# Kernel optimization log

Hardware: AMD Instinct MI355X
Metric: run time of the kernel (lower is better)

Reference implementation:

```python
import jax, jax.numpy as jnp
import numpy as np

B, S, D = 8, 1024, 768
H, DK = 12, 64
DFF = 3072
EPS = 1e-5


def setup_inputs() -> dict:
    key = jax.random.key(0)
    ks = jax.random.split(key, 12)
    s = lambda fan_in: 1.0 / np.sqrt(fan_in)
    return {
        "x": jax.random.normal(ks[0], (B, S, D), jnp.float32),
        "Wq": jax.random.normal(ks[1], (D, D), jnp.float32) * s(D),
        "Wk": jax.random.normal(ks[2], (D, D), jnp.float32) * s(D),
        "Wv": jax.random.normal(ks[3], (D, D), jnp.float32) * s(D),
        "Wo": jax.random.normal(ks[4], (D, D), jnp.float32) * s(D),
        "g1": jnp.ones((D,), jnp.float32),
        "b1": jnp.zeros((D,), jnp.float32),
        "g2": jnp.ones((D,), jnp.float32),
        "b2": jnp.zeros((D,), jnp.float32),
        "W1": jax.random.normal(ks[5], (D, DFF), jnp.float32) * s(D),
        "bW1": jnp.zeros((DFF,), jnp.float32),
        "W2": jax.random.normal(ks[6], (DFF, D), jnp.float32) * s(DFF),
        "bW2": jnp.zeros((D,), jnp.float32),
    }


def _layernorm(x, g, b):
    mu = x.mean(-1, keepdims=True)
    var = ((x - mu) ** 2).mean(-1, keepdims=True)
    return (x - mu) * jax.lax.rsqrt(var + EPS) * g + b


def reference(x, Wq, Wk, Wv, Wo, g1, b1, g2, b2, W1, bW1, W2, bW2):
    scale = DK ** (-0.5)
    # pre-norm attention block
    h = _layernorm(x, g1, b1)
    q = (h @ Wq).reshape(B, S, H, DK)
    k = (h @ Wk).reshape(B, S, H, DK)
    v = (h @ Wv).reshape(B, S, H, DK)
    logits = jnp.einsum("bqhd,bkhd->bhqk", q, k) * scale  # [B,H,S,S]
    weights = jax.nn.softmax(logits, axis=-1)
    attn = jnp.einsum("bhqk,bkhd->bqhd", weights, v).reshape(B, S, D)
    x = x + attn @ Wo
    # pre-norm FFN block
    h = _layernorm(x, g2, b2)
    h = jax.nn.gelu(h @ W1 + bW1, approximate=False)
    x = x + h @ W2 + bW2
    return x
```

## Files before the change

### kernel.cpp

```cpp
#include <hip/hip_runtime.h>
#include <cstdint>
#include <cstddef>

#define B_   8
#define S_   1024
#define D_   768
#define H_   12
#define DK_  64
#define DFF_ 3072
#define M_   (B_*S_)

typedef __attribute__((ext_vector_type(8))) short  short8;
typedef __attribute__((ext_vector_type(4))) short  short4v;
typedef __attribute__((ext_vector_type(8))) __bf16 bf16x8;
typedef __attribute__((ext_vector_type(4))) float  f32x4;
typedef __attribute__((ext_vector_type(4))) unsigned uint4v;
typedef __attribute__((ext_vector_type(2))) unsigned uint2v;

__device__ __forceinline__ unsigned short f2bf(float f) {
    unsigned u = __builtin_bit_cast(unsigned, f);
    u += 0x7FFFu + ((u >> 16) & 1u);
    return (unsigned short)(u >> 16);
}

__device__ __forceinline__ unsigned pkbf(float a, float b) {
    unsigned short ua = __builtin_bit_cast(unsigned short, (__bf16)a);
    unsigned short ub = __builtin_bit_cast(unsigned short, (__bf16)b);
    return (unsigned)ua | ((unsigned)ub << 16);
}

__device__ __forceinline__ f32x4 mfma16(short8 a, short8 b, f32x4 c) {
    return __builtin_amdgcn_mfma_f32_16x16x32_bf16(
        __builtin_bit_cast(bf16x8, a), __builtin_bit_cast(bf16x8, b), c, 0, 0, 0);
}

__device__ __forceinline__ void gload16(const void* g, void* l) {
    auto gp = reinterpret_cast<const __attribute__((address_space(1))) unsigned*>(
        reinterpret_cast<uintptr_t>(g));
    auto lp = reinterpret_cast<__attribute__((address_space(3))) unsigned*>(
        reinterpret_cast<uintptr_t>(l));
    __builtin_amdgcn_global_load_lds(gp, lp, 16, 0, 0);
}

__device__ __forceinline__ float gelu_fast(float v) {
    float w = v * __builtin_fmaf(v * v, 0.044715f, 1.0f);
    float e = __builtin_amdgcn_exp2f(-2.3021178f * w);
    return v * __builtin_amdgcn_rcpf(1.0f + e);
}

__global__ __launch_bounds__(256) void wtrans4_kernel(
    const float* __restrict__ W0, const float* __restrict__ W1,
    const float* __restrict__ W2, const float* __restrict__ W3,
    unsigned short* __restrict__ Wt)
{
    __shared__ float tile[32][33];
    int z = blockIdx.z;
    const float* W = (z == 0) ? W0 : (z == 1) ? W1 : (z == 2) ? W2 : W3;
    unsigned short* dst = Wt + (size_t)z * 768 * 768;
    int n0 = blockIdx.x * 32, k0 = blockIdx.y * 32;
    int tx = threadIdx.x, ty = threadIdx.y;
#pragma unroll
    for (int j = 0; j < 4; ++j)
        tile[ty + j*8][tx] = W[(size_t)(k0 + ty + j*8) * 768 + n0 + tx];
    __syncthreads();
#pragma unroll
    for (int j = 0; j < 4; ++j)
        dst[(size_t)(n0 + ty + j*8) * 768 + k0 + tx] = f2bf(tile[tx][ty + j*8]);
}

__global__ __launch_bounds__(256) void wtrans_kernel(
    const float* __restrict__ W, unsigned short* __restrict__ Wt, int K, int N)
{
    __shared__ float tile[32][33];
    int n0 = blockIdx.x * 32, k0 = blockIdx.y * 32;
    int tx = threadIdx.x, ty = threadIdx.y;
#pragma unroll
    for (int j = 0; j < 4; ++j)
        tile[ty + j*8][tx] = W[(size_t)(k0 + ty + j*8) * N + n0 + tx];
    __syncthreads();
#pragma unroll
    for (int j = 0; j < 4; ++j)
        Wt[(size_t)(n0 + ty + j*8) * K + k0 + tx] = f2bf(tile[tx][ty + j*8]);
}

__global__ __launch_bounds__(256) void ln_kernel(
    const float* __restrict__ x, const float* __restrict__ g,
    const float* __restrict__ b, unsigned short* __restrict__ out)
{
    int row = blockIdx.x, t = threadIdx.x;
    const float* xr = x + (size_t)row * D_;
    float v[3];
#pragma unroll
    for (int i = 0; i < 3; ++i) v[i] = xr[t + i*256];
    float s  = v[0] + v[1] + v[2];
    float ss = v[0]*v[0] + v[1]*v[1] + v[2]*v[2];
#pragma unroll
    for (int d = 1; d < 64; d <<= 1) { s += __shfl_xor(s, d); ss += __shfl_xor(ss, d); }
    __shared__ float red[8];
    int w = t >> 6, lane = t & 63;
    if (lane == 0) { red[w] = s; red[4 + w] = ss; }
    __syncthreads();
    s  = red[0] + red[1] + red[2] + red[3];
    ss = red[4] + red[5] + red[6] + red[7];
    float mu   = s * (1.0f / D_);
    float var  = ss * (1.0f / D_) - mu * mu;
    float rstd = rsqrtf(var + 1e-5f);
    unsigned short* orow = out + (size_t)row * D_;
#pragma unroll
    for (int i = 0; i < 3; ++i) {
        int c = t + i*256;
        orow[c] = f2bf((v[i] - mu) * rstd * g[c] + b[c]);
    }
}

template<int BN, int EPI>
__global__ __launch_bounds__(256, 2) void gemm_kernel(
    const unsigned short* __restrict__ A, const unsigned short* __restrict__ Wt,
    const float* __restrict__ bias, const float* __restrict__ resid,
    void* __restrict__ outp, int N, int K)
{
    __shared__ unsigned short Al[2][128*64];
    __shared__ unsigned short Bl[2][BN*64];
    constexpr int NJ = BN / 64;
    constexpr int ASH = 4, BSH = 2*NJ;
    const int nbn = N / BN;
    const int nwg = gridDim.x;
    const int p = blockIdx.x;
    const int bid = (p & 7) * (nwg >> 3) + (p >> 3);
    const int bm = bid / nbn, bn = bid % nbn;
    const int t = threadIdx.x;
    const int lane = t & 63, w = t >> 6;
    const int wm = w >> 1, wn = w & 1;
    const int lr = lane & 15, lh = lane >> 4;
    const char* aBase = (const char*)(A  + (size_t)(bm*128) * K);
    const char* bBase = (const char*)(Wt + (size_t)(bn*BN)  * K);

    uintptr_t aAdr[ASH], bAdr[BSH];
#pragma unroll
    for (int s = 0; s < ASH; ++s) {
        int d = s*4096 + t*16;
        int row = d >> 7;
        int ch  = ((d >> 4) & 7) ^ (row & 7);
        aAdr[s] = (uintptr_t)aBase + (size_t)row*(K*2) + ch*16;
    }
#pragma unroll
    for (int s = 0; s < BSH; ++s) {
        int d = s*4096 + t*16;
        int row = d >> 7;
        int ch  = ((d >> 4) & 7) ^ (row & 7);
        bAdr[s] = (uintptr_t)bBase + (size_t)row*(K*2) + ch*16;
    }

    f32x4 acc[4][2*NJ] = {};

    auto stage = [&](int kt, int buf) {
        const int k0b = kt << 7;
#pragma unroll
        for (int s = 0; s < ASH; ++s)
            gload16((const void*)(aAdr[s] + k0b), (char*)&Al[buf][0] + s*4096 + t*16);
#pragma unroll
        for (int s = 0; s < BSH; ++s)
            gload16((const void*)(bAdr[s] + k0b), (char*)&Bl[buf][0] + s*4096 + t*16);
    };

    const int nk = K >> 6;
    stage(0, 0);
    stage(1, 1);

    for (int it = 0; it < nk; ++it) {
        const int buf = it & 1;
        if (it + 1 < nk) {
            if constexpr (BN == 128) asm volatile("s_waitcnt vmcnt(8)" ::: "memory");
            else                     asm volatile("s_waitcnt vmcnt(6)" ::: "memory");
        } else {
            asm volatile("s_waitcnt vmcnt(0)" ::: "memory");
        }
        __builtin_amdgcn_s_barrier();

        short8 xf[2][4], wf[2][2*NJ];
#pragma unroll
        for (int kk = 0; kk < 2; ++kk) {
#pragma unroll
            for (int i = 0; i < 4; ++i)
                xf[kk][i] = *reinterpret_cast<const short8*>(
                    &Al[buf][(wm*64 + i*16 + lr)*64 + (((kk*4 + lh) ^ (lr & 7))*8)]);
#pragma unroll
            for (int j = 0; j < 2*NJ; ++j)
                wf[kk][j] = *reinterpret_cast<const short8*>(
                    &Bl[buf][(wn*(32*NJ) + j*16 + lr)*64 + (((kk*4 + lh) ^ (lr & 7))*8)]);
        }
        __builtin_amdgcn_s_setprio(1);
#pragma unroll
        for (int kk = 0; kk < 2; ++kk)
#pragma unroll
            for (int i = 0; i < 4; ++i)
#pragma unroll
                for (int j = 0; j < 2*NJ; ++j)
                    acc[i][j] = mfma16(wf[kk][j], xf[kk][i], acc[i][j]);
        __builtin_amdgcn_s_setprio(0);
        __builtin_amdgcn_s_barrier();
        if (it + 2 < nk) stage(it + 2, buf);
    }

#pragma unroll
    for (int i = 0; i < 4; ++i) {
        const int m = bm*128 + wm*64 + i*16 + lr;
#pragma unroll
        for (int j = 0; j < 2*NJ; ++j) {
            const int n0 = bn*BN + wn*(32*NJ) + j*16 + lh*4;
            f32x4 v = acc[i][j];
            if (EPI == 1) {
                f32x4 bb = *reinterpret_cast<const f32x4*>(&bias[n0]);
                v += bb;
#pragma unroll
                for (int r = 0; r < 4; ++r) v[r] = gelu_fast(v[r]);
            }
            if (EPI == 2) {
                if (bias) v += *reinterpret_cast<const f32x4*>(&bias[n0]);
                v += *reinterpret_cast<const f32x4*>(&resid[(size_t)m*N + n0]);
                *reinterpret_cast<f32x4*>(&((float*)outp)[(size_t)m*N + n0]) = v;
            } else {
                uint2v pv = { pkbf(v[0], v[1]), pkbf(v[2], v[3]) };
                *reinterpret_cast<uint2v*>(&((unsigned short*)outp)[(size_t)m*N + n0]) = pv;
            }
        }
    }
}

__global__ __launch_bounds__(256) void vtrans_kernel(
    const unsigned short* __restrict__ qkv, unsigned short* __restrict__ vt)
{
    __shared__ unsigned short tl[64][65];
    int bid = blockIdx.x;
    int sblk = bid & 15, bh = bid >> 4;
    int b = bh / H_, h = bh % H_;
    int t = threadIdx.x, tx = t & 63, ty = t >> 6;
    int s0 = sblk * 64;
#pragma unroll
    for (int j = 0; j < 16; ++j) {
        int s = j*4 + ty;
        tl[s][tx] = qkv[(size_t)(b*S_ + s0 + s)*2304 + 1536 + h*64 + tx];
    }
    __syncthreads();
#pragma unroll
    for (int j = 0; j < 16; ++j) {
        int dk = j*4 + ty;
        vt[((size_t)bh*64 + dk)*S_ + s0 + tx] = tl[tx][dk];
    }
}

__global__ __launch_bounds__(256, 3) void attn_kernel(
    const unsigned short* __restrict__ qkv, const unsigned short* __restrict__ vt,
    unsigned short* __restrict__ out)
{
    __shared__ unsigned short Kl[2][64*64];
    __shared__ unsigned short Vl[2][64*64];

    const int p = blockIdx.x;
    const int l = (p & 7) * 96 + (p >> 3);
    const int qb = l & 7, bh = l >> 3;
    const int b = bh / H_, h = bh % H_;
    const int t = threadIdx.x, lane = t & 63, w = t >> 6;
    const int lr = lane & 15, lh = lane >> 4;
    const int sz = (lr & 7) << 3;

    const float SC = 0.125f * 1.44269504089f;
    const float SHIFT = 12.0f;

    const int qrow0 = qb*128 + w*32;
    short8 bq[2][2];
#pragma unroll
    for (int qi = 0; qi < 2; ++qi) {
        const unsigned short* qp = qkv + (size_t)(b*S_ + qrow0 + qi*16 + lr)*2304 + h*64;
#pragma unroll
        for (int c = 0; c < 2; ++c)
            bq[qi][c] = *reinterpret_cast<const short8*>(&qp[c*32 + lh*8]);
    }

    float l_run[2] = {0.f, 0.f};
    f32x4 o[2][4] = {};

    uintptr_t kAdr[2], vAdr[2];
#pragma unroll
    for (int shot = 0; shot < 2; ++shot) {
        int d = shot*4096 + t*16;
        int row = d >> 7;
        int sc = (d & 127) ^ ((row & 7) << 4);
        kAdr[shot] = (uintptr_t)qkv + ((size_t)(b*S_ + row)*2304 + 768 + h*64)*2 + sc;
        vAdr[shot] = (uintptr_t)vt  + ((size_t)(bh*64 + row)*1024)*2 + sc;
    }

    auto stage = [&](int kb, int buf) {
        const size_t kOff = (size_t)kb * 64 * 2304 * 2;
        const size_t vOff = (size_t)kb * 128;
#pragma unroll
        for (int shot = 0; shot < 2; ++shot) {
            int d = shot*4096 + t*16;
            gload16((const void*)(kAdr[shot] + kOff), (char*)&Kl[buf][0] + d);
            gload16((const void*)(vAdr[shot] + vOff), (char*)&Vl[buf][0] + d);
        }
    };

    stage(0, 0);
    asm volatile("s_waitcnt vmcnt(0)" ::: "memory");
    __builtin_amdgcn_s_barrier();

    for (int kb = 0; kb < 16; ++kb) {
        const int buf = kb & 1;
        if (kb < 15) stage(kb + 1, buf ^ 1);

        short8 ak[4][2];
#pragma unroll
        for (int j = 0; j < 4; ++j)
#pragma unroll
            for (int c = 0; c < 2; ++c)
                ak[j][c] = *reinterpret_cast<const short8*>(
                    &Kl[buf][(j*16 + lr)*64 + ((c*32 + lh*8) ^ sz)]);

        short8 av[4][2];
#pragma unroll
        for (int j = 0; j < 4; ++j) {
            const unsigned short* vrow = &Vl[buf][(j*16 + lr)*64];
#pragma unroll
            for (int ks = 0; ks < 2; ++ks) {
                short4v lo = *reinterpret_cast<const short4v*>(&vrow[(ks*32 + lh*4)      ^ sz]);
                short4v hi = *reinterpret_cast<const short4v*>(&vrow[(ks*32 + 16 + lh*4) ^ sz]);
                av[j][ks] = __builtin_shufflevector(lo, hi, 0,1,2,3,4,5,6,7);
            }
        }

#pragma unroll
        for (int qi = 0; qi < 2; ++qi) {
            f32x4 s[4];
            __builtin_amdgcn_s_setprio(1);
#pragma unroll
            for (int j = 0; j < 4; ++j) {
                f32x4 z = {0.f, 0.f, 0.f, 0.f};
                z = mfma16(ak[j][0], bq[qi][0], z);
                z = mfma16(ak[j][1], bq[qi][1], z);
                s[j] = z;
            }
            __builtin_amdgcn_s_setprio(0);

            float rs = 0.f;
#pragma unroll
            for (int j = 0; j < 4; ++j)
#pragma unroll
                for (int r = 0; r < 4; ++r) {
                    float pv = __builtin_amdgcn_exp2f(
                        __builtin_fmaf(s[j][r], SC, -SHIFT));
                    s[j][r] = pv;
                    rs += pv;
                }
            l_run[qi] += rs;

            uint4v u0 = { pkbf(s[0][0], s[0][1]), pkbf(s[0][2], s[0][3]),
                          pkbf(s[1][0], s[1][1]), pkbf(s[1][2], s[1][3]) };
            uint4v u1 = { pkbf(s[2][0], s[2][1]), pkbf(s[2][2], s[2][3]),
                          pkbf(s[3][0], s[3][1]), pkbf(s[3][2], s[3][3]) };
            short8 pb0 = __builtin_bit_cast(short8, u0);
            short8 pb1 = __builtin_bit_cast(short8, u1);

            __builtin_amdgcn_s_setprio(1);
#pragma unroll
            for (int j = 0; j < 4; ++j) {
                o[qi][j] = mfma16(av[j][0], pb0, o[qi][j]);
                o[qi][j] = mfma16(av[j][1], pb1, o[qi][j]);
            }
            __builtin_amdgcn_s_setprio(0);
        }

        asm volatile("s_waitcnt vmcnt(0)" ::: "memory");
        __builtin_amdgcn_s_barrier();
    }

#pragma unroll
    for (int qi = 0; qi < 2; ++qi) {
        float ls = l_run[qi];
        ls += __shfl_xor(ls, 16);
        ls += __shfl_xor(ls, 32);
        float inv = 1.0f / ls;
        int q = qrow0 + qi*16 + lr;
        unsigned short* orow = out + (size_t)(b*S_ + q)*D_ + h*64;
#pragma unroll
        for (int j = 0; j < 4; ++j) {
            uint2v vv = { pkbf(o[qi][j][0]*inv, o[qi][j][1]*inv),
                          pkbf(o[qi][j][2]*inv, o[qi][j][3]*inv) };
            *reinterpret_cast<uint2v*>(&orow[j*16 + lh*4]) = vv;
        }
    }
}

extern "C" void kernel_launch(void* const* d_in, const int* in_sizes, int n_in,
                              void* d_out, int out_size, void* d_ws, size_t ws_size,
                              hipStream_t stream)
{
    (void)in_sizes; (void)n_in; (void)out_size; (void)ws_size;
    const float* x   = (const float*)d_in[0];
    const float* Wq  = (const float*)d_in[1];
    const float* Wk  = (const float*)d_in[2];
    const float* Wv  = (const float*)d_in[3];
    const float* Wo  = (const float*)d_in[4];
    const float* g1  = (const float*)d_in[5];
    const float* b1  = (const float*)d_in[6];
    const float* g2  = (const float*)d_in[7];
    const float* b2  = (const float*)d_in[8];
    const float* W1  = (const float*)d_in[9];
    const float* bW1 = (const float*)d_in[10];
    const float* W2  = (const float*)d_in[11];
    const float* bW2 = (const float*)d_in[12];
    float* out = (float*)d_out;

    char* ws = (char*)d_ws;
    unsigned short* wt_qkv = (unsigned short*)(ws);
    unsigned short* wt_o   = (unsigned short*)(ws + 3538944);
    unsigned short* wt_1   = (unsigned short*)(ws + 4718592);
    unsigned short* wt_2   = (unsigned short*)(ws + 9437184);
    unsigned short* slotA  = (unsigned short*)(ws + 14155776);
    unsigned short* qkv    = (unsigned short*)(ws + 26738688);
    unsigned short* vt     = (unsigned short*)(ws + 64487424);
    unsigned short* ffm    = qkv;

    dim3 tb(32, 8);
    wtrans4_kernel<<<dim3(24,24,4), tb, 0, stream>>>(Wq, Wk, Wv, Wo, wt_qkv);
    wtrans_kernel<<<dim3(96,24), tb, 0, stream>>>(W1, wt_1, 768, 3072);
    wtrans_kernel<<<dim3(24,96), tb, 0, stream>>>(W2, wt_2, 3072, 768);

    ln_kernel<<<M_, 256, 0, stream>>>(x, g1, b1, slotA);
    gemm_kernel<128,0><<<1152, 256, 0, stream>>>(slotA, wt_qkv, nullptr, nullptr, qkv, 2304, 768);
    vtrans_kernel<<<1536, 256, 0, stream>>>(qkv, vt);
    attn_kernel<<<768, 256, 0, stream>>>(qkv, vt, slotA);
    gemm_kernel<64,2><<<768, 256, 0, stream>>>(slotA, wt_o, nullptr, x, (void*)out, 768, 768);
    ln_kernel<<<M_, 256, 0, stream>>>(out, g2, b2, slotA);
    gemm_kernel<128,1><<<1536, 256, 0, stream>>>(slotA, wt_1, bW1, nullptr, ffm, 3072, 768);
    gemm_kernel<64,2><<<768, 256, 0, stream>>>(ffm, wt_2, bW2, out, (void*)out, 768, 3072);
}
```

Baseline: 261.0 us.

## Use 128x64 GEMM tiles with triple-buffered LDS and XCD-aware tile mapping

The GEMM kernel now always uses a 128x64 output tile and is templated on pipeline depth. The QKV and FFN1 GEMMs get triple-buffered LDS staging with adjusted vmcnt waits, and the grid doubles to match. Block-to-tile mapping is rewritten so each XCD owns contiguous row blocks split into two column halves, aiming for better L2 reuse per XCD. Smaller N tiles reload A more often and halve MFMA work per barrier, traded against deeper prefetch and more workgroups.

```diff
diff --git a/kernel.cpp b/kernel.cpp
--- a/kernel.cpp
+++ b/kernel.cpp
@@ -113,27 +113,32 @@
     }
 }
 
-template<int BN, int EPI>
+template<int DEPTH, int EPI>
 __global__ __launch_bounds__(256, 2) void gemm_kernel(
     const unsigned short* __restrict__ A, const unsigned short* __restrict__ Wt,
     const float* __restrict__ bias, const float* __restrict__ resid,
     void* __restrict__ outp, int N, int K)
 {
-    __shared__ unsigned short Al[2][128*64];
-    __shared__ unsigned short Bl[2][BN*64];
-    constexpr int NJ = BN / 64;
-    constexpr int ASH = 4, BSH = 2*NJ;
-    const int nbn = N / BN;
+    __shared__ unsigned short Al[DEPTH][128*64];
+    __shared__ unsigned short Bl[DEPTH][64*64];
+    constexpr int ASH = 4, BSH = 2;
     const int nwg = gridDim.x;
     const int p = blockIdx.x;
-    const int bid = (p & 7) * (nwg >> 3) + (p >> 3);
-    const int bm = bid / nbn, bn = bid % nbn;
+    const int cpx = nwg >> 3;
+    const int xcd = p & 7, id = p >> 3;
+    const int nbn = N >> 6;
+    const int rows = cpx / nbn;
+    const int hn = nbn >> 1, hc = cpx >> 1;
+    const int half = id / hc, r = id % hc;
+    const int bm = xcd * rows + r / hn;
+    const int bn = half * hn + r % hn;
+
     const int t = threadIdx.x;
     const int lane = t & 63, w = t >> 6;
     const int wm = w >> 1, wn = w & 1;
     const int lr = lane & 15, lh = lane >> 4;
     const char* aBase = (const char*)(A  + (size_t)(bm*128) * K);
-    const char* bBase = (const char*)(Wt + (size_t)(bn*BN)  * K);
+    const char* bBase = (const char*)(Wt + (size_t)(bn*64)  * K);
 
     uintptr_t aAdr[ASH], bAdr[BSH];
 #pragma unroll
@@ -151,7 +156,7 @@
         bAdr[s] = (uintptr_t)bBase + (size_t)row*(K*2) + ch*16;
     }
 
-    f32x4 acc[4][2*NJ] = {};
+    f32x4 acc[4][2] = {};
 
     auto stage = [&](int kt, int buf) {
         const int k0b = kt << 7;
@@ -166,18 +171,21 @@
     const int nk = K >> 6;
     stage(0, 0);
     stage(1, 1);
-
+    if constexpr (DEPTH == 3) stage(2, 2);
+
+    int buf = 0;
     for (int it = 0; it < nk; ++it) {
-        const int buf = it & 1;
-        if (it + 1 < nk) {
-            if constexpr (BN == 128) asm volatile("s_waitcnt vmcnt(8)" ::: "memory");
-            else                     asm volatile("s_waitcnt vmcnt(6)" ::: "memory");
+        if constexpr (DEPTH == 3) {
+            if (it < nk - 2)       asm volatile("s_waitcnt vmcnt(12)" ::: "memory");
+            else if (it == nk - 2) asm volatile("s_waitcnt vmcnt(6)"  ::: "memory");
+            else                   asm volatile("s_waitcnt vmcnt(0)"  ::: "memory");
         } else {
-            asm volatile("s_waitcnt vmcnt(0)" ::: "memory");
+            if (it + 1 < nk)       asm volatile("s_waitcnt vmcnt(6)"  ::: "memory");
+            else                   asm volatile("s_waitcnt vmcnt(0)"  ::: "memory");
         }
         __builtin_amdgcn_s_barrier();
 
-        short8 xf[2][4], wf[2][2*NJ];
+        short8 xf[2][4], wf[2][2];
 #pragma unroll
         for (int kk = 0; kk < 2; ++kk) {
 #pragma unroll
@@ -185,9 +193,9 @@
                 xf[kk][i] = *reinterpret_cast<const short8*>(
                     &Al[buf][(wm*64 + i*16 + lr)*64 + (((kk*4 + lh) ^ (lr & 7))*8)]);
 #pragma unroll
-            for (int j = 0; j < 2*NJ; ++j)
+            for (int j = 0; j < 2; ++j)
                 wf[kk][j] = *reinterpret_cast<const short8*>(
-                    &Bl[buf][(wn*(32*NJ) + j*16 + lr)*64 + (((kk*4 + lh) ^ (lr & 7))*8)]);
+                    &Bl[buf][(wn*32 + j*16 + lr)*64 + (((kk*4 + lh) ^ (lr & 7))*8)]);
         }
         __builtin_amdgcn_s_setprio(1);
 #pragma unroll
@@ -195,25 +203,26 @@
 #pragma unroll
             for (int i = 0; i < 4; ++i)
 #pragma unroll
-                for (int j = 0; j < 2*NJ; ++j)
+                for (int j = 0; j < 2; ++j)
                     acc[i][j] = mfma16(wf[kk][j], xf[kk][i], acc[i][j]);
         __builtin_amdgcn_s_setprio(0);
         __builtin_amdgcn_s_barrier();
-        if (it + 2 < nk) stage(it + 2, buf);
+        if (it + DEPTH < nk) stage(it + DEPTH, buf);
+        buf = (buf + 1 == DEPTH) ? 0 : buf + 1;
     }
 
 #pragma unroll
     for (int i = 0; i < 4; ++i) {
         const int m = bm*128 + wm*64 + i*16 + lr;
 #pragma unroll
-        for (int j = 0; j < 2*NJ; ++j) {
-            const int n0 = bn*BN + wn*(32*NJ) + j*16 + lh*4;
+        for (int j = 0; j < 2; ++j) {
+            const int n0 = bn*64 + wn*32 + j*16 + lh*4;
             f32x4 v = acc[i][j];
             if (EPI == 1) {
                 f32x4 bb = *reinterpret_cast<const f32x4*>(&bias[n0]);
                 v += bb;
 #pragma unroll
-                for (int r = 0; r < 4; ++r) v[r] = gelu_fast(v[r]);
+                for (int r2 = 0; r2 < 4; ++r2) v[r2] = gelu_fast(v[r2]);
             }
             if (EPI == 2) {
                 if (bias) v += *reinterpret_cast<const f32x4*>(&bias[n0]);
@@ -427,11 +436,11 @@
     wtrans_kernel<<<dim3(24,96), tb, 0, stream>>>(W2, wt_2, 3072, 768);
 
     ln_kernel<<<M_, 256, 0, stream>>>(x, g1, b1, slotA);
-    gemm_kernel<128,0><<<1152, 256, 0, stream>>>(slotA, wt_qkv, nullptr, nullptr, qkv, 2304, 768);
+    gemm_kernel<3,0><<<2304, 256, 0, stream>>>(slotA, wt_qkv, nullptr, nullptr, qkv, 2304, 768);
     vtrans_kernel<<<1536, 256, 0, stream>>>(qkv, vt);
     attn_kernel<<<768, 256, 0, stream>>>(qkv, vt, slotA);
-    gemm_kernel<64,2><<<768, 256, 0, stream>>>(slotA, wt_o, nullptr, x, (void*)out, 768, 768);
+    gemm_kernel<2,2><<<768, 256, 0, stream>>>(slotA, wt_o, nullptr, x, (void*)out, 768, 768);
     ln_kernel<<<M_, 256, 0, stream>>>(out, g2, b2, slotA);
-    gemm_kernel<128,1><<<1536, 256, 0, stream>>>(slotA, wt_1, bW1, nullptr, ffm, 3072, 768);
-    gemm_kernel<64,2><<<768, 256, 0, stream>>>(ffm, wt_2, bW2, out, (void*)out, 768, 3072);
-}
+    gemm_kernel<3,1><<<3072, 256, 0, stream>>>(slotA, wt_1, bW1, nullptr, ffm, 3072, 768);
+    gemm_kernel<2,2><<<768, 256, 0, stream>>>(ffm, wt_2, bW2, out, (void*)out, 768, 3072);
+}
```

Result: slower. 266.5 us (+2.1%).
